# Kernel tuning notes

Hardware: AMD Instinct MI355X
Metric: run time of the kernel (lower is better)

Reference implementation:

```python
import jax, jax.numpy as jnp
import numpy as np

N_NODES = 50000
N_EDGES = 800000
IN_C, HID_C, LAT_C = 128, 64, 32
DEC_HID, REC_C = 64, 128


def _glorot(key, shape):
    fan_in, fan_out = shape
    lim = jnp.sqrt(6.0 / (fan_in + fan_out))
    return jax.random.uniform(key, shape, jnp.float32, -lim, lim)


def setup_inputs() -> dict:
    key = jax.random.key(0)
    ks = jax.random.split(key, 8)
    x = jax.random.normal(ks[0], (N_NODES, IN_C), jnp.float32)
    edge_index = jax.random.randint(ks[1], (2, N_EDGES), 0, N_NODES, jnp.int64 if jax.config.jax_enable_x64 else jnp.int32)
    return {
        "x": x,
        "edge_index": edge_index,
        "W_e1": _glorot(ks[2], (IN_C, HID_C)), "b_e1": jnp.zeros((HID_C,), jnp.float32),
        "W_e2": _glorot(ks[3], (HID_C, LAT_C)), "b_e2": jnp.zeros((LAT_C,), jnp.float32),
        "W_d1": _glorot(ks[4], (LAT_C, DEC_HID)), "b_d1": jnp.zeros((DEC_HID,), jnp.float32),
        "W_d2": _glorot(ks[5], (DEC_HID, REC_C)), "b_d2": jnp.zeros((REC_C,), jnp.float32),
    }


def _gcn_conv(x, src, dst, dinv, W, b, n_nodes):
    # GCNConv: h = D^{-1/2} (A + I) D^{-1/2} (x W) + b, expressed over the edge list
    h = x @ W                                   # [N, out]
    norm = dinv[src] * dinv[dst]                # [E+N] symmetric normalization
    msg = h[src] * norm[:, None]                # gather + per-edge scale (memory-bound)
    out = jax.ops.segment_sum(msg, dst, num_segments=n_nodes)  # scatter-add
    return out + b


def reference(x, edge_index, W_e1, b_e1, W_e2, b_e2, W_d1, b_d1, W_d2, b_d2):
    n = x.shape[0]
    loops = jnp.arange(n, dtype=edge_index.dtype)
    src = jnp.concatenate([edge_index[0], loops])
    dst = jnp.concatenate([edge_index[1], loops])
    # degree (with self-loops) computed once; deg >= 1 so rsqrt is safe
    deg = jax.ops.segment_sum(jnp.ones_like(src, dtype=x.dtype), dst, num_segments=n)
    dinv = jax.lax.rsqrt(deg)

    # encoder (dropout is eval-mode identity)
    h = jax.nn.relu(_gcn_conv(x, src, dst, dinv, W_e1, b_e1, n))
    z = _gcn_conv(h, src, dst, dinv, W_e2, b_e2, n)           # latent embeddings
    # decoder mirrors GCNConv layers
    d = jax.nn.relu(_gcn_conv(z, src, dst, dinv, W_d1, b_d1, n))
    x_rec = _gcn_conv(d, src, dst, dinv, W_d2, b_d2, n)       # [N, reconstructed_feature_dim]
    return x_rec
```

## Files before the change

### kernel.cpp

```cpp
#include <hip/hip_runtime.h>

typedef _Float16 half4 __attribute__((ext_vector_type(4)));
typedef _Float16 half8 __attribute__((ext_vector_type(8)));


static constexpr int NPB_SHIFT = 6;
static constexpr int NPB = 1 << NPB_SHIFT;
static constexpr int MAX_BKT = 1024;
static constexpr int PS_CHUNK = 4096;

__global__ __launch_bounds__(256) void hist_kernel(const int* __restrict__ dst, int E,
                                                   int nbkt, int* __restrict__ hist) {
    __shared__ int lc[MAX_BKT];
    int tid = threadIdx.x;
    int b = blockIdx.x;
    int e0 = b * PS_CHUNK;
    int e1 = e0 + PS_CHUNK; if (e1 > E) e1 = E;
    for (int i = tid; i < nbkt; i += 256) lc[i] = 0;
    __syncthreads();
    for (int i = e0 + tid; i < e1; i += 256)
        atomicAdd(&lc[dst[i] >> NPB_SHIFT], 1);
    __syncthreads();
    for (int i = tid; i < nbkt; i += 256) hist[(size_t)b * nbkt + i] = lc[i];
}

__global__ __launch_bounds__(256) void col_scan_kernel(int* __restrict__ hist, int nchunk,
                                                       int nbkt, int* __restrict__ bcnt) {
    int i = blockIdx.x * 4 + (threadIdx.x >> 6);
    if (i >= nbkt) return;
    int lane = threadIdx.x & 63;
    int run = 0;
    for (int c0 = 0; c0 < nchunk; c0 += 64) {
        int c = c0 + lane;
        int v = (c < nchunk) ? hist[(size_t)c * nbkt + i] : 0;
        int inc = v;
#pragma unroll
        for (int m = 1; m < 64; m <<= 1) {
            int u = __shfl_up(inc, m);
            if (lane >= m) inc += u;
        }
        if (c < nchunk) hist[(size_t)c * nbkt + i] = run + inc - v;
        run += __shfl(inc, 63);
    }
    if (lane == 0) bcnt[i] = run;
}

__global__ __launch_bounds__(256) void bucket_scan_kernel(const int* __restrict__ bcnt, int nbkt,
                                                          int* __restrict__ bbase,
                                                          int* __restrict__ rowp, int n) {
    __shared__ int wsum[4];
    int tid = threadIdx.x, lane = tid & 63, w = tid >> 6;
    int chunk = (nbkt + 255) / 256;
    int begin = tid * chunk;
    int end = begin + chunk; if (end > nbkt) end = nbkt;
    int s = 0;
    for (int i = begin; i < end; ++i) s += bcnt[i];
    int inc = s;
#pragma unroll
    for (int m = 1; m < 64; m <<= 1) {
        int u = __shfl_up(inc, m);
        if (lane >= m) inc += u;
    }
    if (lane == 63) wsum[w] = inc;
    __syncthreads();
    int off = 0;
    for (int i = 0; i < w; ++i) off += wsum[i];
    int run = off + inc - s;
    for (int i = begin; i < end; ++i) {
        bbase[i] = run;
        run += bcnt[i];
    }
    if (tid == 255) { bbase[nbkt] = run; rowp[n] = run; }
}

__global__ __launch_bounds__(256) void pair_blocksort_kernel(const int* __restrict__ src,
                                                             const int* __restrict__ dst,
                                                             int E, int nbkt,
                                                             const int* __restrict__ hist,
                                                             const int* __restrict__ bbase,
                                                             int* __restrict__ part) {
    __shared__ int2 pairs[PS_CHUNK];
    __shared__ int lbase[MAX_BKT];
    __shared__ int lcur[MAX_BKT];
    __shared__ int gpos[MAX_BKT];
    __shared__ int wsum[4];
    const int tid = threadIdx.x;
    const int b = blockIdx.x;
    const int e0 = b * PS_CHUNK;
    int e1 = e0 + PS_CHUNK; if (e1 > E) e1 = E;

    for (int i = tid; i < nbkt; i += 256) {
        lcur[i] = 0;
        gpos[i] = bbase[i] + hist[(size_t)b * nbkt + i];
    }
    __syncthreads();
    for (int i = e0 + tid; i < e1; i += 256)
        atomicAdd(&lcur[dst[i] >> NPB_SHIFT], 1);
    __syncthreads();
    {
        int b0 = tid * 4;
        int v[4]; int s = 0;
#pragma unroll
        for (int k = 0; k < 4; ++k) {
            int bb = b0 + k;
            v[k] = (bb < nbkt) ? lcur[bb] : 0;
            s += v[k];
        }
        int lane = tid & 63, w = tid >> 6;
        int inc = s;
#pragma unroll
        for (int m = 1; m < 64; m <<= 1) {
            int u = __shfl_up(inc, m);
            if (lane >= m) inc += u;
        }
        if (lane == 63) wsum[w] = inc;
        __syncthreads();
        int off = 0;
        for (int i = 0; i < w; ++i) off += wsum[i];
        int run = off + inc - s;
        __syncthreads();
#pragma unroll
        for (int k = 0; k < 4; ++k) {
            int bb = b0 + k;
            if (bb < nbkt) { lbase[bb] = run; lcur[bb] = run; }
            run += v[k];
        }
    }
    __syncthreads();
    for (int i = e0 + tid; i < e1; i += 256) {
        int s = src[i], d = dst[i];
        int p = atomicAdd(&lcur[d >> NPB_SHIFT], 1);
        pairs[p] = make_int2(s, d);
    }
    __syncthreads();
    const int cnt = e1 - e0;
    for (int i = tid; i < cnt; i += 256) {
        int2 pr = pairs[i];
        int bk = pr.y >> NPB_SHIFT;
        part[gpos[bk] + (i - lbase[bk])] = (pr.x << NPB_SHIFT) | (pr.y & (NPB - 1));
    }
}


template <bool HALF>
__device__ __forceinline__ float4 ldrow4(const void* H, size_t off) {
    if constexpr (HALF) {
        half4 h = *reinterpret_cast<const half4*>(reinterpret_cast<const _Float16*>(H) + off);
        return make_float4((float)h.x, (float)h.y, (float)h.z, (float)h.w);
    } else {
        return *reinterpret_cast<const float4*>(reinterpret_cast<const float*>(H) + off);
    }
}

template <bool HALF>
__device__ __forceinline__ void strow4(void* H, size_t off, float4 o) {
    if constexpr (HALF) {
        half4 hv;
        hv.x = (_Float16)o.x; hv.y = (_Float16)o.y;
        hv.z = (_Float16)o.z; hv.w = (_Float16)o.w;
        *reinterpret_cast<half4*>(reinterpret_cast<_Float16*>(H) + off) = hv;
    } else {
        *reinterpret_cast<float4*>(reinterpret_cast<float*>(H) + off) = o;
    }
}

__global__ __launch_bounds__(256) void csr_g1_kernel(
        const int* __restrict__ part, const int* __restrict__ bbase, int n,
        int* __restrict__ rowp, float* __restrict__ dinv, int* __restrict__ csr,
        const float* __restrict__ X, const float* __restrict__ We1,
        void* __restrict__ H1) {
    __shared__ int lcnt[NPB];
    __shared__ float sdinv[NPB];
    __shared__ __align__(16) char smem[50176];
    const int b = blockIdx.x, tid = threadIdx.x;
    const int node0 = b << NPB_SHIFT;
    int nloc = n - node0; if (nloc > NPB) nloc = NPB;
    const int p0 = bbase[b], p1 = bbase[b + 1];

    if (tid < NPB) lcnt[tid] = 0;
    __syncthreads();
    for (int i = p0 + tid; i < p1; i += 256)
        atomicAdd(&lcnt[part[i] & (NPB - 1)], 1);
    __syncthreads();
    if (tid < 64) {
        int c = lcnt[tid];
        int inc = c;
#pragma unroll
        for (int m = 1; m < 64; m <<= 1) {
            int u = __shfl_up(inc, m);
            if (tid >= m) inc += u;
        }
        int base = p0 + inc - c;
        float dv = rsqrtf((float)(c + 1));
        if (tid < nloc) {
            rowp[node0 + tid] = base;
            dinv[node0 + tid] = dv;
        }
        sdinv[tid] = dv;
        lcnt[tid] = base;
    }
    __syncthreads();
    for (int i = p0 + tid; i < p1; i += 256) {
        int w = part[i];
        int pos = atomicAdd(&lcnt[w & (NPB - 1)], 1);
        csr[pos] = w >> NPB_SHIFT;
    }
    __syncthreads();

    float (*At)[68] = reinterpret_cast<float (*)[68]>(smem);
    float (*Bl)[64] = reinterpret_cast<float (*)[64]>(smem + 17408);
    const int tx = tid % 16, ty = tid / 16;

    for (int i = tid; i < 128 * 16; i += 256) {
        int k = i / 16, c4 = (i % 16) * 4;
        *reinterpret_cast<float4*>(&Bl[k][c4]) =
            *reinterpret_cast<const float4*>(&We1[(size_t)k * 64 + c4]);
    }

    float acc[4][4] = {};
#pragma unroll
    for (int ch = 0; ch < 2; ++ch) {
        if (ch) __syncthreads();
        for (int i = tid; i < 64 * 16; i += 256) {
            int r = i / 16, k0 = (i % 16) * 4;
            int rg = node0 + r; if (rg > n - 1) rg = n - 1;
            float4 xv = *reinterpret_cast<const float4*>(&X[(size_t)rg * 128 + ch * 64 + k0]);
            At[k0 + 0][r] = xv.x;
            At[k0 + 1][r] = xv.y;
            At[k0 + 2][r] = xv.z;
            At[k0 + 3][r] = xv.w;
        }
        __syncthreads();
#pragma unroll 8
        for (int k = 0; k < 64; ++k) {
            float4 a = *reinterpret_cast<const float4*>(&At[k][ty * 4]);
            float4 bb = *reinterpret_cast<const float4*>(&Bl[ch * 64 + k][tx * 4]);
            acc[0][0] = fmaf(a.x, bb.x, acc[0][0]); acc[0][1] = fmaf(a.x, bb.y, acc[0][1]);
            acc[0][2] = fmaf(a.x, bb.z, acc[0][2]); acc[0][3] = fmaf(a.x, bb.w, acc[0][3]);
            acc[1][0] = fmaf(a.y, bb.x, acc[1][0]); acc[1][1] = fmaf(a.y, bb.y, acc[1][1]);
            acc[1][2] = fmaf(a.y, bb.z, acc[1][2]); acc[1][3] = fmaf(a.y, bb.w, acc[1][3]);
            acc[2][0] = fmaf(a.z, bb.x, acc[2][0]); acc[2][1] = fmaf(a.z, bb.y, acc[2][1]);
            acc[2][2] = fmaf(a.z, bb.z, acc[2][2]); acc[2][3] = fmaf(a.z, bb.w, acc[2][3]);
            acc[3][0] = fmaf(a.w, bb.x, acc[3][0]); acc[3][1] = fmaf(a.w, bb.y, acc[3][1]);
            acc[3][2] = fmaf(a.w, bb.z, acc[3][2]); acc[3][3] = fmaf(a.w, bb.w, acc[3][3]);
        }
    }
#pragma unroll
    for (int i = 0; i < 4; ++i) {
        int r = ty * 4 + i;
        int nd = node0 + r;
        if (nd < n) {
            float dv = sdinv[r];
            float4 o = make_float4(acc[i][0] * dv, acc[i][1] * dv,
                                   acc[i][2] * dv, acc[i][3] * dv);
            strow4<true>(H1, (size_t)nd * 64 + tx * 4, o);
        }
    }
}

template <int K, int OUT, int BN, bool BIAS, bool RELU, bool SCALE, bool HALF_IN, bool HALF_OUT>
__global__ __launch_bounds__(16 * (BN / 4)) void gemm_tile_kernel(
        const void* __restrict__ X, const float* __restrict__ W,
        const float* __restrict__ bias, const float* __restrict__ dinv,
        void* __restrict__ Hout, int n) {
    constexpr int BM = 64;
    constexpr int KB = (K > 64) ? 64 : K;
    constexpr int NTHR = 16 * (BN / 4);
    constexpr int KV = KB / 4;

    __shared__ float At[KB][BM + 4];
    __shared__ float Bl[K][BN];

    const int tid = threadIdx.x;
    const int tx = tid % (BN / 4);
    const int ty = tid / (BN / 4);
    const int rb = blockIdx.x * BM;
    const int co = blockIdx.y * BN;

    for (int i = tid; i < K * BN / 4; i += NTHR) {
        int k = i / (BN / 4);
        int c0 = (i % (BN / 4)) * 4;
        *reinterpret_cast<float4*>(&Bl[k][c0]) =
            *reinterpret_cast<const float4*>(&W[(size_t)k * OUT + co + c0]);
    }

    float acc[4][4] = {};

#pragma unroll
    for (int ch = 0; ch < K / KB; ++ch) {
        if (ch) __syncthreads();
        for (int i = tid; i < BM * KV; i += NTHR) {
            int r = i / KV;
            int k0 = (i % KV) * 4;
            int rg = rb + r; if (rg > n - 1) rg = n - 1;
            float4 xv = ldrow4<HALF_IN>(X, (size_t)rg * K + ch * KB + k0);
            At[k0 + 0][r] = xv.x;
            At[k0 + 1][r] = xv.y;
            At[k0 + 2][r] = xv.z;
            At[k0 + 3][r] = xv.w;
        }
        __syncthreads();

#pragma unroll 8
        for (int k = 0; k < KB; ++k) {
            float4 a = *reinterpret_cast<const float4*>(&At[k][ty * 4]);
            float4 b = *reinterpret_cast<const float4*>(&Bl[ch * KB + k][tx * 4]);
            acc[0][0] = fmaf(a.x, b.x, acc[0][0]); acc[0][1] = fmaf(a.x, b.y, acc[0][1]);
            acc[0][2] = fmaf(a.x, b.z, acc[0][2]); acc[0][3] = fmaf(a.x, b.w, acc[0][3]);
            acc[1][0] = fmaf(a.y, b.x, acc[1][0]); acc[1][1] = fmaf(a.y, b.y, acc[1][1]);
            acc[1][2] = fmaf(a.y, b.z, acc[1][2]); acc[1][3] = fmaf(a.y, b.w, acc[1][3]);
            acc[2][0] = fmaf(a.z, b.x, acc[2][0]); acc[2][1] = fmaf(a.z, b.y, acc[2][1]);
            acc[2][2] = fmaf(a.z, b.z, acc[2][2]); acc[2][3] = fmaf(a.z, b.w, acc[2][3]);
            acc[3][0] = fmaf(a.w, b.x, acc[3][0]); acc[3][1] = fmaf(a.w, b.y, acc[3][1]);
            acc[3][2] = fmaf(a.w, b.z, acc[3][2]); acc[3][3] = fmaf(a.w, b.w, acc[3][3]);
        }
    }

    float4 bv = make_float4(0.f, 0.f, 0.f, 0.f);
    if (BIAS) bv = *reinterpret_cast<const float4*>(&bias[co + tx * 4]);
    int r0 = rb + ty * 4;
#pragma unroll
    for (int i = 0; i < 4; ++i) {
        int r = r0 + i;
        if (r < n) {
            float4 o;
            o.x = acc[i][0]; o.y = acc[i][1]; o.z = acc[i][2]; o.w = acc[i][3];
            if (BIAS) { o.x += bv.x; o.y += bv.y; o.z += bv.z; o.w += bv.w; }
            if (RELU) {
                o.x = fmaxf(o.x, 0.f); o.y = fmaxf(o.y, 0.f);
                o.z = fmaxf(o.z, 0.f); o.w = fmaxf(o.w, 0.f);
            }
            if (SCALE) {
                float dv = dinv[r];
                o.x *= dv; o.y *= dv; o.z *= dv; o.w *= dv;
            }
            strow4<HALF_OUT>(Hout, (size_t)r * OUT + co + tx * 4, o);
        }
    }
}

template <int C, bool RELU, bool HAS_BIAS, bool POST_SCALE>
__global__ __launch_bounds__(256) void aggregate_kernel(const _Float16* __restrict__ H,
                                                        const int* __restrict__ row,
                                                        const int* __restrict__ csr_src,
                                                        const float* __restrict__ dinv,
                                                        const float* __restrict__ bias,
                                                        _Float16* __restrict__ Y, int n) {
    constexpr int LPN = C / 8;
    constexpr int EG = 64 / LPN;
    int wid = (blockIdx.x * blockDim.x + threadIdx.x) >> 6;
    if (wid >= n) return;
    int lane = threadIdx.x & 63;
    int g = lane / LPN;
    int c0 = (lane % LPN) * 8;
    const int node = wid;

    float accA[8] = {};
    float accB[8] = {};
    if (g == 0) {
        half8 h = *reinterpret_cast<const half8*>(H + (size_t)node * C + c0);
#pragma unroll
        for (int j = 0; j < 8; ++j) accA[j] = (float)h[j];
    }
    int e = row[node] + g;
    const int end = row[node + 1];
    for (; e + EG < end; e += 2 * EG) {
        int s0 = csr_src[e];
        int s1 = csr_src[e + EG];
        half8 h0 = *reinterpret_cast<const half8*>(H + (size_t)s0 * C + c0);
        half8 h1 = *reinterpret_cast<const half8*>(H + (size_t)s1 * C + c0);
#pragma unroll
        for (int j = 0; j < 8; ++j) { accA[j] += (float)h0[j]; accB[j] += (float)h1[j]; }
    }
    if (e < end) {
        int s = csr_src[e];
        half8 h = *reinterpret_cast<const half8*>(H + (size_t)s * C + c0);
#pragma unroll
        for (int j = 0; j < 8; ++j) accA[j] += (float)h[j];
    }
#pragma unroll
    for (int j = 0; j < 8; ++j) accA[j] += accB[j];
#pragma unroll
    for (int m = LPN; m < 64; m <<= 1) {
#pragma unroll
        for (int j = 0; j < 8; ++j) accA[j] += __shfl_xor(accA[j], m);
    }
    if (g == 0) {
        float dv = dinv[node];
        half8 o;
#pragma unroll
        for (int j = 0; j < 8; ++j) {
            float v = accA[j] * dv;
            if (HAS_BIAS) v += bias[c0 + j];
            if (RELU) v = fmaxf(v, 0.f);
            if (POST_SCALE) v *= dv;
            o[j] = (_Float16)v;
        }
        *reinterpret_cast<half8*>(Y + (size_t)node * C + c0) = o;
    }
}


static inline int cdiv(int a, int b) { return (a + b - 1) / b; }

extern "C" void kernel_launch(void* const* d_in, const int* in_sizes, int n_in,
                              void* d_out, int out_size, void* d_ws, size_t ws_size,
                              hipStream_t stream) {
    const float* x   = (const float*)d_in[0];
    const int*   ei  = (const int*)d_in[1];
    const float* We1 = (const float*)d_in[2];
    const float* be1 = (const float*)d_in[3];
    const float* We2 = (const float*)d_in[4];
    const float* be2 = (const float*)d_in[5];
    const float* Wd1 = (const float*)d_in[6];
    const float* bd1 = (const float*)d_in[7];
    const float* Wd2 = (const float*)d_in[8];
    const float* bd2 = (const float*)d_in[9];

    const int n = in_sizes[0] / 128;
    const int E = in_sizes[1] / 2;
    const int* src = ei;
    const int* dst = ei + E;
    const int nbkt = cdiv(n, NPB);
    const int nchunk = cdiv(E, PS_CHUNK);
    const int nrb = cdiv(n, 64);
    const int nwv = cdiv(n * 64, 256);

    char* ws = (char*)d_ws;
    auto carve = [&](size_t bytes) -> void* {
        void* p = (void*)ws;
        ws += (bytes + 255) & ~(size_t)255;
        return p;
    };
    int*   hist = (int*)carve((size_t)nchunk * nbkt * 4);
    int*   bcnt = (int*)carve((size_t)nbkt * 4);
    int*   bbase= (int*)carve((size_t)(nbkt + 1) * 4);
    int*   part = (int*)carve((size_t)E * 4);
    int*   rowp = (int*)carve((size_t)(n + 1) * 4);
    float* dinv = (float*)carve((size_t)n * 4);
    int*   csr  = (int*)carve((size_t)E * 4);
    _Float16* P1 = (_Float16*)carve((size_t)n * 64 * 2);
    _Float16* P2 = (_Float16*)carve((size_t)n * 64 * 2);
    _Float16* P3 = (_Float16*)carve((size_t)n * 32 * 2);
    _Float16* P4 = (_Float16*)carve((size_t)n * 32 * 2);

    hist_kernel<<<nchunk, 256, 0, stream>>>(dst, E, nbkt, hist);
    col_scan_kernel<<<cdiv(nbkt, 4), 256, 0, stream>>>(hist, nchunk, nbkt, bcnt);
    bucket_scan_kernel<<<1, 256, 0, stream>>>(bcnt, nbkt, bbase, rowp, n);
    pair_blocksort_kernel<<<nchunk, 256, 0, stream>>>(src, dst, E, nbkt, hist, bbase, part);

    csr_g1_kernel<<<nbkt, 256, 0, stream>>>(part, bbase, n, rowp, dinv, csr, x, We1, P1);

    aggregate_kernel<64, true, true, false>
        <<<nwv, 256, 0, stream>>>(P1, rowp, csr, dinv, be1, P2, n);

    gemm_tile_kernel<64, 32, 32, false, false, true, true, true>
        <<<dim3(nrb, 1), 128, 0, stream>>>(P2, We2, nullptr, dinv, P3, n);

    aggregate_kernel<32, false, true, true>
        <<<nwv, 256, 0, stream>>>(P3, rowp, csr, dinv, be2, P4, n);

    aggregate_kernel<32, false, false, false>
        <<<nwv, 256, 0, stream>>>(P4, rowp, csr, dinv, nullptr, P3, n);

    gemm_tile_kernel<32, 64, 64, true, true, true, true, true>
        <<<dim3(nrb, 1), 256, 0, stream>>>(P3, Wd1, bd1, dinv, P1, n);

    aggregate_kernel<64, false, false, false>
        <<<nwv, 256, 0, stream>>>(P1, rowp, csr, dinv, nullptr, P2, n);

    gemm_tile_kernel<64, 128, 64, true, false, false, true, false>
        <<<dim3(nrb, 2), 256, 0, stream>>>(P2, Wd2, bd2, dinv, d_out, n);
}
```

Baseline: 184.2 us.

## Fuse neighbor aggregation with following dense layer matmul per node

```diff
diff --git a/kernel.cpp b/kernel.cpp
--- a/kernel.cpp
+++ b/kernel.cpp
@@ -143,16 +143,6 @@
 
 
 template <bool HALF>
-__device__ __forceinline__ float4 ldrow4(const void* H, size_t off) {
-    if constexpr (HALF) {
-        half4 h = *reinterpret_cast<const half4*>(reinterpret_cast<const _Float16*>(H) + off);
-        return make_float4((float)h.x, (float)h.y, (float)h.z, (float)h.w);
-    } else {
-        return *reinterpret_cast<const float4*>(reinterpret_cast<const float*>(H) + off);
-    }
-}
-
-template <bool HALF>
 __device__ __forceinline__ void strow4(void* H, size_t off, float4 o) {
     if constexpr (HALF) {
         half4 hv;
@@ -254,87 +244,6 @@
             float4 o = make_float4(acc[i][0] * dv, acc[i][1] * dv,
                                    acc[i][2] * dv, acc[i][3] * dv);
             strow4<true>(H1, (size_t)nd * 64 + tx * 4, o);
-        }
-    }
-}
-
-template <int K, int OUT, int BN, bool BIAS, bool RELU, bool SCALE, bool HALF_IN, bool HALF_OUT>
-__global__ __launch_bounds__(16 * (BN / 4)) void gemm_tile_kernel(
-        const void* __restrict__ X, const float* __restrict__ W,
-        const float* __restrict__ bias, const float* __restrict__ dinv,
-        void* __restrict__ Hout, int n) {
-    constexpr int BM = 64;
-    constexpr int KB = (K > 64) ? 64 : K;
-    constexpr int NTHR = 16 * (BN / 4);
-    constexpr int KV = KB / 4;
-
-    __shared__ float At[KB][BM + 4];
-    __shared__ float Bl[K][BN];
-
-    const int tid = threadIdx.x;
-    const int tx = tid % (BN / 4);
-    const int ty = tid / (BN / 4);
-    const int rb = blockIdx.x * BM;
-    const int co = blockIdx.y * BN;
-
-    for (int i = tid; i < K * BN / 4; i += NTHR) {
-        int k = i / (BN / 4);
-        int c0 = (i % (BN / 4)) * 4;
-        *reinterpret_cast<float4*>(&Bl[k][c0]) =
-            *reinterpret_cast<const float4*>(&W[(size_t)k * OUT + co + c0]);
-    }
-
-    float acc[4][4] = {};
-
-#pragma unroll
-    for (int ch = 0; ch < K / KB; ++ch) {
-        if (ch) __syncthreads();
-        for (int i = tid; i < BM * KV; i += NTHR) {
-            int r = i / KV;
-            int k0 = (i % KV) * 4;
-            int rg = rb + r; if (rg > n - 1) rg = n - 1;
-            float4 xv = ldrow4<HALF_IN>(X, (size_t)rg * K + ch * KB + k0);
-            At[k0 + 0][r] = xv.x;
-            At[k0 + 1][r] = xv.y;
-            At[k0 + 2][r] = xv.z;
-            At[k0 + 3][r] = xv.w;
-        }
-        __syncthreads();
-
-#pragma unroll 8
-        for (int k = 0; k < KB; ++k) {
-            float4 a = *reinterpret_cast<const float4*>(&At[k][ty * 4]);
-            float4 b = *reinterpret_cast<const float4*>(&Bl[ch * KB + k][tx * 4]);
-            acc[0][0] = fmaf(a.x, b.x, acc[0][0]); acc[0][1] = fmaf(a.x, b.y, acc[0][1]);
-            acc[0][2] = fmaf(a.x, b.z, acc[0][2]); acc[0][3] = fmaf(a.x, b.w, acc[0][3]);
-            acc[1][0] = fmaf(a.y, b.x, acc[1][0]); acc[1][1] = fmaf(a.y, b.y, acc[1][1]);
-            acc[1][2] = fmaf(a.y, b.z, acc[1][2]); acc[1][3] = fmaf(a.y, b.w, acc[1][3]);
-            acc[2][0] = fmaf(a.z, b.x, acc[2][0]); acc[2][1] = fmaf(a.z, b.y, acc[2][1]);
-            acc[2][2] = fmaf(a.z, b.z, acc[2][2]); acc[2][3] = fmaf(a.z, b.w, acc[2][3]);
-            acc[3][0] = fmaf(a.w, b.x, acc[3][0]); acc[3][1] = fmaf(a.w, b.y, acc[3][1]);
-            acc[3][2] = fmaf(a.w, b.z, acc[3][2]); acc[3][3] = fmaf(a.w, b.w, acc[3][3]);
-        }
-    }
-
-    float4 bv = make_float4(0.f, 0.f, 0.f, 0.f);
-    if (BIAS) bv = *reinterpret_cast<const float4*>(&bias[co + tx * 4]);
-    int r0 = rb + ty * 4;
-#pragma unroll
-    for (int i = 0; i < 4; ++i) {
-        int r = r0 + i;
-        if (r < n) {
-            float4 o;
-            o.x = acc[i][0]; o.y = acc[i][1]; o.z = acc[i][2]; o.w = acc[i][3];
-            if (BIAS) { o.x += bv.x; o.y += bv.y; o.z += bv.z; o.w += bv.w; }
-            if (RELU) {
-                o.x = fmaxf(o.x, 0.f); o.y = fmaxf(o.y, 0.f);
-                o.z = fmaxf(o.z, 0.f); o.w = fmaxf(o.w, 0.f);
-            }
-            if (SCALE) {
-                float dv = dinv[r];
-                o.x *= dv; o.y *= dv; o.z *= dv; o.w *= dv;
-            }
-            strow4<HALF_OUT>(Hout, (size_t)r * OUT + co + tx * 4, o);
         }
     }
 }
@@ -400,6 +309,140 @@
     }
 }
 
+template <int CIN, int COUT, bool A_BIAS, bool A_RELU,
+          bool B_BIAS, bool B_RELU, bool B_SCALE, bool OUT_HALF>
+__global__ __launch_bounds__(256) void agg_mv_kernel(
+        const _Float16* __restrict__ H, const int* __restrict__ row,
+        const int* __restrict__ csr_src, const float* __restrict__ dinv,
+        const float* __restrict__ abias, const float* __restrict__ W,
+        const float* __restrict__ bbias, void* __restrict__ Out, int n) {
+    constexpr int LPN = CIN / 8;
+    constexpr int EG = 64 / LPN;
+    constexpr int WPAD = CIN + 8;
+    __shared__ __align__(16) _Float16 Wl[COUT][WPAD];
+    __shared__ __align__(16) _Float16 rowbuf[4][CIN];
+
+    const int tid = threadIdx.x;
+    for (int i = tid; i < CIN * COUT; i += 256) {
+        int k = i / COUT, c = i % COUT;
+        Wl[c][k] = (_Float16)W[(size_t)k * COUT + c];
+    }
+    __syncthreads();
+
+    const int wv = tid >> 6, lane = tid & 63;
+    const int node = blockIdx.x * 4 + wv;
+    if (node >= n) return;
+    const int g = lane / LPN;
+    const int c0 = (lane % LPN) * 8;
+
+    float accA[8] = {};
+    float accB[8] = {};
+    if (g == 0) {
+        half8 h = *reinterpret_cast<const half8*>(H + (size_t)node * CIN + c0);
+#pragma unroll
+        for (int j = 0; j < 8; ++j) accA[j] = (float)h[j];
+    }
+    int e = row[node] + g;
+    const int end = row[node + 1];
+    for (; e + EG < end; e += 2 * EG) {
+        int s0 = csr_src[e];
+        int s1 = csr_src[e + EG];
+        half8 h0 = *reinterpret_cast<const half8*>(H + (size_t)s0 * CIN + c0);
+        half8 h1 = *reinterpret_cast<const half8*>(H + (size_t)s1 * CIN + c0);
+#pragma unroll
+        for (int j = 0; j < 8; ++j) { accA[j] += (float)h0[j]; accB[j] += (float)h1[j]; }
+    }
+    if (e < end) {
+        int s = csr_src[e];
+        half8 h = *reinterpret_cast<const half8*>(H + (size_t)s * CIN + c0);
+#pragma unroll
+        for (int j = 0; j < 8; ++j) accA[j] += (float)h[j];
+    }
+#pragma unroll
+    for (int j = 0; j < 8; ++j) accA[j] += accB[j];
+#pragma unroll
+    for (int m = LPN; m < 64; m <<= 1) {
+#pragma unroll
+        for (int j = 0; j < 8; ++j) accA[j] += __shfl_xor(accA[j], m);
+    }
+
+    const float dv = dinv[node];
+    if (g == 0) {
+        half8 o;
+#pragma unroll
+        for (int j = 0; j < 8; ++j) {
+            float v = accA[j] * dv;
+            if (A_BIAS) v += abias[c0 + j];
+            if (A_RELU) v = fmaxf(v, 0.f);
+            o[j] = (_Float16)v;
+        }
+        *reinterpret_cast<half8*>(&rowbuf[wv][c0]) = o;
+    }
+    const _Float16* rb = rowbuf[wv];
+
+    if constexpr (COUT == 32) {
+        const int c = lane & 31, kh = lane >> 5;
+        float acc = 0.f;
+#pragma unroll
+        for (int kb = 0; kb < CIN / 16; ++kb) {
+            half8 r8 = *reinterpret_cast<const half8*>(rb + kh * (CIN / 2) + kb * 8);
+            half8 w8 = *reinterpret_cast<const half8*>(&Wl[c][kh * (CIN / 2) + kb * 8]);
+#pragma unroll
+            for (int j = 0; j < 8; ++j) acc = fmaf((float)r8[j], (float)w8[j], acc);
+        }
+        acc += __shfl_xor(acc, 32);
+        if (lane < 32) {
+            float v = acc;
+            if (B_BIAS) v += bbias[c];
+            if (B_RELU) v = fmaxf(v, 0.f);
+            if (B_SCALE) v *= dv;
+            if (OUT_HALF) ((_Float16*)Out)[(size_t)node * COUT + c] = (_Float16)v;
+            else          ((float*)Out)[(size_t)node * COUT + c] = v;
+        }
+    } else if constexpr (COUT == 64) {
+        const int c = lane;
+        float acc = 0.f;
+#pragma unroll
+        for (int kb = 0; kb < CIN / 8; ++kb) {
+            half8 r8 = *reinterpret_cast<const half8*>(rb + kb * 8);
+            half8 w8 = *reinterpret_cast<const half8*>(&Wl[c][kb * 8]);
+#pragma unroll
+            for (int j = 0; j < 8; ++j) acc = fmaf((float)r8[j], (float)w8[j], acc);
+        }
+        float v = acc;
+        if (B_BIAS) v += bbias[c];
+        if (B_RELU) v = fmaxf(v, 0.f);
+        if (B_SCALE) v *= dv;
+        if (OUT_HALF) ((_Float16*)Out)[(size_t)node * COUT + c] = (_Float16)v;
+        else          ((float*)Out)[(size_t)node * COUT + c] = v;
+    } else {
+        const int ca = lane, cb = lane + 64;
+        float a0 = 0.f, a1 = 0.f;
+#pragma unroll
+        for (int kb = 0; kb < CIN / 8; ++kb) {
+            half8 r8 = *reinterpret_cast<const half8*>(rb + kb * 8);
+            half8 w0 = *reinterpret_cast<const half8*>(&Wl[ca][kb * 8]);
+            half8 w1 = *reinterpret_cast<const half8*>(&Wl[cb][kb * 8]);
+#pragma unroll
+            for (int j = 0; j < 8; ++j) {
+                a0 = fmaf((float)r8[j], (float)w0[j], a0);
+                a1 = fmaf((float)r8[j], (float)w1[j], a1);
+            }
+        }
+        float v0 = a0, v1 = a1;
+        if (B_BIAS) { v0 += bbias[ca]; v1 += bbias[cb]; }
+        if (B_RELU) { v0 = fmaxf(v0, 0.f); v1 = fmaxf(v1, 0.f); }
+        if (B_SCALE) { v0 *= dv; v1 *= dv; }
+        if (OUT_HALF) {
+            ((_Float16*)Out)[(size_t)node * COUT + ca] = (_Float16)v0;
+            ((_Float16*)Out)[(size_t)node * COUT + cb] = (_Float16)v1;
+        } else {
+            ((float*)Out)[(size_t)node * COUT + ca] = v0;
+            ((float*)Out)[(size_t)node * COUT + cb] = v1;
+        }
+    }
+}
+
 
 static inline int cdiv(int a, int b) { return (a + b - 1) / b; }
 
@@ -423,8 +466,7 @@
     const int* dst = ei + E;
     const int nbkt = cdiv(n, NPB);
     const int nchunk = cdiv(E, PS_CHUNK);
-    const int nrb = cdiv(n, 64);
-    const int nwv = cdiv(n * 64, 256);
+    const int nwb = cdiv(n, 4);
 
     char* ws = (char*)d_ws;
     auto carve = [&](size_t bytes) -> void* {
@@ -440,7 +482,6 @@
     float* dinv = (float*)carve((size_t)n * 4);
     int*   csr  = (int*)carve((size_t)E * 4);
     _Float16* P1 = (_Float16*)carve((size_t)n * 64 * 2);
-    _Float16* P2 = (_Float16*)carve((size_t)n * 64 * 2);
     _Float16* P3 = (_Float16*)carve((size_t)n * 32 * 2);
     _Float16* P4 = (_Float16*)carve((size_t)n * 32 * 2);
 
@@ -451,24 +492,15 @@
 
     csr_g1_kernel<<<nbkt, 256, 0, stream>>>(part, bbase, n, rowp, dinv, csr, x, We1, P1);
 
-    aggregate_kernel<64, true, true, false>
-        <<<nwv, 256, 0, stream>>>(P1, rowp, csr, dinv, be1, P2, n);
-
-    gemm_tile_kernel<64, 32, 32, false, false, true, true, true>
-        <<<dim3(nrb, 1), 128, 0, stream>>>(P2, We2, nullptr, dinv, P3, n);
+    agg_mv_kernel<64, 32, true, true, false, false, true, true>
+        <<<nwb, 256, 0, stream>>>(P1, rowp, csr, dinv, be1, We2, nullptr, P3, n);
 
     aggregate_kernel<32, false, true, true>
-        <<<nwv, 256, 0, stream>>>(P3, rowp, csr, dinv, be2, P4, n);
-
-    aggregate_kernel<32, false, false, false>
-        <<<nwv, 256, 0, stream>>>(P4, rowp, csr, dinv, nullptr, P3, n);
-
-    gemm_tile_kernel<32, 64, 64, true, true, true, true, true>
-        <<<dim3(nrb, 1), 256, 0, stream>>>(P3, Wd1, bd1, dinv, P1, n);
-
-    aggregate_kernel<64, false, false, false>
-        <<<nwv, 256, 0, stream>>>(P1, rowp, csr, dinv, nullptr, P2, n);
-
-    gemm_tile_kernel<64, 128, 64, true, false, false, true, false>
-        <<<dim3(nrb, 2), 256, 0, stream>>>(P2, Wd2, bd2, dinv, d_out, n);
-}
+        <<<cdiv(n * 64, 256), 256, 0, stream>>>(P3, rowp, csr, dinv, be2, P4, n);
+
+    agg_mv_kernel<32, 64, false, false, true, true, true, true>
+        <<<nwb, 256, 0, stream>>>(P4, rowp, csr, dinv, nullptr, Wd1, bd1, P1, n);
+
+    agg_mv_kernel<64, 128, false, false, true, false, false, false>
+        <<<nwb, 256, 0, stream>>>(P1, rowp, csr, dinv, nullptr, Wd2, bd2, d_out, n);
+}
```

Result: slower. 201.2 us (+9.2%).

## Fuse neighbor aggregation with following small dense transform per node

Applied to the files above, without the earlier changes.

```diff
diff --git a/kernel.cpp b/kernel.cpp
--- a/kernel.cpp
+++ b/kernel.cpp
@@ -143,16 +143,6 @@
 
 
 template <bool HALF>
-__device__ __forceinline__ float4 ldrow4(const void* H, size_t off) {
-    if constexpr (HALF) {
-        half4 h = *reinterpret_cast<const half4*>(reinterpret_cast<const _Float16*>(H) + off);
-        return make_float4((float)h.x, (float)h.y, (float)h.z, (float)h.w);
-    } else {
-        return *reinterpret_cast<const float4*>(reinterpret_cast<const float*>(H) + off);
-    }
-}
-
-template <bool HALF>
 __device__ __forceinline__ void strow4(void* H, size_t off, float4 o) {
     if constexpr (HALF) {
         half4 hv;
@@ -254,87 +244,6 @@
             float4 o = make_float4(acc[i][0] * dv, acc[i][1] * dv,
                                    acc[i][2] * dv, acc[i][3] * dv);
             strow4<true>(H1, (size_t)nd * 64 + tx * 4, o);
-        }
-    }
-}
-
-template <int K, int OUT, int BN, bool BIAS, bool RELU, bool SCALE, bool HALF_IN, bool HALF_OUT>
-__global__ __launch_bounds__(16 * (BN / 4)) void gemm_tile_kernel(
-        const void* __restrict__ X, const float* __restrict__ W,
-        const float* __restrict__ bias, const float* __restrict__ dinv,
-        void* __restrict__ Hout, int n) {
-    constexpr int BM = 64;
-    constexpr int KB = (K > 64) ? 64 : K;
-    constexpr int NTHR = 16 * (BN / 4);
-    constexpr int KV = KB / 4;
-
-    __shared__ float At[KB][BM + 4];
-    __shared__ float Bl[K][BN];
-
-    const int tid = threadIdx.x;
-    const int tx = tid % (BN / 4);
-    const int ty = tid / (BN / 4);
-    const int rb = blockIdx.x * BM;
-    const int co = blockIdx.y * BN;
-
-    for (int i = tid; i < K * BN / 4; i += NTHR) {
-        int k = i / (BN / 4);
-        int c0 = (i % (BN / 4)) * 4;
-        *reinterpret_cast<float4*>(&Bl[k][c0]) =
-            *reinterpret_cast<const float4*>(&W[(size_t)k * OUT + co + c0]);
-    }
-
-    float acc[4][4] = {};
-
-#pragma unroll
-    for (int ch = 0; ch < K / KB; ++ch) {
-        if (ch) __syncthreads();
-        for (int i = tid; i < BM * KV; i += NTHR) {
-            int r = i / KV;
-            int k0 = (i % KV) * 4;
-            int rg = rb + r; if (rg > n - 1) rg = n - 1;
-            float4 xv = ldrow4<HALF_IN>(X, (size_t)rg * K + ch * KB + k0);
-            At[k0 + 0][r] = xv.x;
-            At[k0 + 1][r] = xv.y;
-            At[k0 + 2][r] = xv.z;
-            At[k0 + 3][r] = xv.w;
-        }
-        __syncthreads();
-
-#pragma unroll 8
-        for (int k = 0; k < KB; ++k) {
-            float4 a = *reinterpret_cast<const float4*>(&At[k][ty * 4]);
-            float4 b = *reinterpret_cast<const float4*>(&Bl[ch * KB + k][tx * 4]);
-            acc[0][0] = fmaf(a.x, b.x, acc[0][0]); acc[0][1] = fmaf(a.x, b.y, acc[0][1]);
-            acc[0][2] = fmaf(a.x, b.z, acc[0][2]); acc[0][3] = fmaf(a.x, b.w, acc[0][3]);
-            acc[1][0] = fmaf(a.y, b.x, acc[1][0]); acc[1][1] = fmaf(a.y, b.y, acc[1][1]);
-            acc[1][2] = fmaf(a.y, b.z, acc[1][2]); acc[1][3] = fmaf(a.y, b.w, acc[1][3]);
-            acc[2][0] = fmaf(a.z, b.x, acc[2][0]); acc[2][1] = fmaf(a.z, b.y, acc[2][1]);
-            acc[2][2] = fmaf(a.z, b.z, acc[2][2]); acc[2][3] = fmaf(a.z, b.w, acc[2][3]);
-            acc[3][0] = fmaf(a.w, b.x, acc[3][0]); acc[3][1] = fmaf(a.w, b.y, acc[3][1]);
-            acc[3][2] = fmaf(a.w, b.z, acc[3][2]); acc[3][3] = fmaf(a.w, b.w, acc[3][3]);
-        }
-    }
-
-    float4 bv = make_float4(0.f, 0.f, 0.f, 0.f);
-    if (BIAS) bv = *reinterpret_cast<const float4*>(&bias[co + tx * 4]);
-    int r0 = rb + ty * 4;
-#pragma unroll
-    for (int i = 0; i < 4; ++i) {
-        int r = r0 + i;
-        if (r < n) {
-            float4 o;
-            o.x = acc[i][0]; o.y = acc[i][1]; o.z = acc[i][2]; o.w = acc[i][3];
-            if (BIAS) { o.x += bv.x; o.y += bv.y; o.z += bv.z; o.w += bv.w; }
-            if (RELU) {
-                o.x = fmaxf(o.x, 0.f); o.y = fmaxf(o.y, 0.f);
-                o.z = fmaxf(o.z, 0.f); o.w = fmaxf(o.w, 0.f);
-            }
-            if (SCALE) {
-                float dv = dinv[r];
-                o.x *= dv; o.y *= dv; o.z *= dv; o.w *= dv;
-            }
-            strow4<HALF_OUT>(Hout, (size_t)r * OUT + co + tx * 4, o);
         }
     }
 }
@@ -400,6 +309,188 @@
     }
 }
 
+template <int CIN, int COUT, bool SPLITK, bool A_BIAS, bool A_RELU,
+          bool B_BIAS, bool B_RELU, bool B_SCALE>
+__global__ __launch_bounds__(256) void agg_mv_kernel(
+        const _Float16* __restrict__ H, const int* __restrict__ row,
+        const int* __restrict__ csr_src, const float* __restrict__ dinv,
+        const float* __restrict__ abias, const float* __restrict__ W,
+        const float* __restrict__ bbias, _Float16* __restrict__ Out, int n) {
+    constexpr int LPN = CIN / 8;
+    constexpr int EG = 64 / LPN;
+    __shared__ float Wf[CIN * COUT];
+    __shared__ float rowbuf[4][CIN];
+
+    const int tid = threadIdx.x;
+    for (int i = tid; i < CIN * COUT / 4; i += 256)
+        *reinterpret_cast<float4*>(&Wf[i * 4]) =
+            *reinterpret_cast<const float4*>(&W[i * 4]);
+    __syncthreads();
+
+    const int wv = tid >> 6, lane = tid & 63;
+    const int node = blockIdx.x * 4 + wv;
+    if (node >= n) return;
+    const int g = lane / LPN;
+    const int c0 = (lane % LPN) * 8;
+
+    float accA[8] = {};
+    float accB[8] = {};
+    if (g == 0) {
+        half8 h = *reinterpret_cast<const half8*>(H + (size_t)node * CIN + c0);
+#pragma unroll
+        for (int j = 0; j < 8; ++j) accA[j] = (float)h[j];
+    }
+    int e = row[node] + g;
+    const int end = row[node + 1];
+    for (; e + EG < end; e += 2 * EG) {
+        int s0 = csr_src[e];
+        int s1 = csr_src[e + EG];
+        half8 h0 = *reinterpret_cast<const half8*>(H + (size_t)s0 * CIN + c0);
+        half8 h1 = *reinterpret_cast<const half8*>(H + (size_t)s1 * CIN + c0);
+#pragma unroll
+        for (int j = 0; j < 8; ++j) { accA[j] += (float)h0[j]; accB[j] += (float)h1[j]; }
+    }
+    if (e < end) {
+        int s = csr_src[e];
+        half8 h = *reinterpret_cast<const half8*>(H + (size_t)s * CIN + c0);
+#pragma unroll
+        for (int j = 0; j < 8; ++j) accA[j] += (float)h[j];
+    }
+#pragma unroll
+    for (int j = 0; j < 8; ++j) accA[j] += accB[j];
+#pragma unroll
+    for (int m = LPN; m < 64; m <<= 1) {
+#pragma unroll
+        for (int j = 0; j < 8; ++j) accA[j] += __shfl_xor(accA[j], m);
+    }
+
+    const float dv = dinv[node];
+    if (g == 0) {
+        float4 lo, hi;
+        float v[8];
+#pragma unroll
+        for (int j = 0; j < 8; ++j) {
+            float t = accA[j] * dv;
+            if (A_BIAS) t += abias[c0 + j];
+            if (A_RELU) t = fmaxf(t, 0.f);
+            v[j] = t;
+        }
+        lo = make_float4(v[0], v[1], v[2], v[3]);
+        hi = make_float4(v[4], v[5], v[6], v[7]);
+        *reinterpret_cast<float4*>(&rowbuf[wv][c0]) = lo;
+        *reinterpret_cast<float4*>(&rowbuf[wv][c0 + 4]) = hi;
+    }
+    const float* rb = rowbuf[wv];
+
+    if constexpr (SPLITK) {
+        const int c = lane & 31, kh = lane >> 5;
+        float acc = 0.f;
+#pragma unroll
+        for (int k = 0; k < CIN / 2; ++k)
+            acc = fmaf(rb[kh * (CIN / 2) + k], Wf[(kh * (CIN / 2) + k) * COUT + c], acc);
+        acc += __shfl_xor(acc, 32);
+        if (lane < 32) {
+            float v = acc;
+            if (B_BIAS) v += bbias[c];
+            if (B_RELU) v = fmaxf(v, 0.f);
+            if (B_SCALE) v *= dv;
+            Out[(size_t)node * COUT + c] = (_Float16)v;
+        }
+    } else {
+        const int c = lane;
+        float acc = 0.f;
+#pragma unroll
+        for (int k = 0; k < CIN; ++k)
+            acc = fmaf(rb[k], Wf[k * COUT + c], acc);
+        float v = acc;
+        if (B_BIAS) v += bbias[c];
+        if (B_RELU) v = fmaxf(v, 0.f);
+        if (B_SCALE) v *= dv;
+        Out[(size_t)node * COUT + c] = (_Float16)v;
+    }
+}
+
+template <int K, int OUT, int BN, bool BIAS, bool RELU, bool SCALE>
+__global__ __launch_bounds__(16 * (BN / 4)) void gemm_tile_kernel(
+        const _Float16* __restrict__ X, const float* __restrict__ W,
+        const float* __restrict__ bias, const float* __restrict__ dinv,
+        float* __restrict__ Hout, int n) {
+    constexpr int BM = 64;
+    constexpr int KB = (K > 64) ? 64 : K;
+    constexpr int NTHR = 16 * (BN / 4);
+    constexpr int KV = KB / 4;
+
+    __shared__ float At[KB][BM + 4];
+    __shared__ float Bl[K][BN];
+
+    const int tid = threadIdx.x;
+    const int tx = tid % (BN / 4);
+    const int ty = tid / (BN / 4);
+    const int rb = blockIdx.x * BM;
+    const int co = blockIdx.y * BN;
+
+    for (int i = tid; i < K * BN / 4; i += NTHR) {
+        int k = i / (BN / 4);
+        int c0 = (i % (BN / 4)) * 4;
+        *reinterpret_cast<float4*>(&Bl[k][c0]) =
+            *reinterpret_cast<const float4*>(&W[(size_t)k * OUT + co + c0]);
+    }
+
+    float acc[4][4] = {};
+
+#pragma unroll
+    for (int ch = 0; ch < K / KB; ++ch) {
+        if (ch) __syncthreads();
+        for (int i = tid; i < BM * KV; i += NTHR) {
+            int r = i / KV;
+            int k0 = (i % KV) * 4;
+            int rg = rb + r; if (rg > n - 1) rg = n - 1;
+            half4 hv = *reinterpret_cast<const half4*>(&X[(size_t)rg * K + ch * KB + k0]);
+            At[k0 + 0][r] = (float)hv.x;
+            At[k0 + 1][r] = (float)hv.y;
+            At[k0 + 2][r] = (float)hv.z;
+            At[k0 + 3][r] = (float)hv.w;
+        }
+        __syncthreads();
+
+#pragma unroll 8
+        for (int k = 0; k < KB; ++k) {
+            float4 a = *reinterpret_cast<const float4*>(&At[k][ty * 4]);
+            float4 b = *reinterpret_cast<const float4*>(&Bl[ch * KB + k][tx * 4]);
+            acc[0][0] = fmaf(a.x, b.x, acc[0][0]); acc[0][1] = fmaf(a.x, b.y, acc[0][1]);
+            acc[0][2] = fmaf(a.x, b.z, acc[0][2]); acc[0][3] = fmaf(a.x, b.w, acc[0][3]);
+            acc[1][0] = fmaf(a.y, b.x, acc[1][0]); acc[1][1] = fmaf(a.y, b.y, acc[1][1]);
+            acc[1][2] = fmaf(a.y, b.z, acc[1][2]); acc[1][3] = fmaf(a.y, b.w, acc[1][3]);
+            acc[2][0] = fmaf(a.z, b.x, acc[2][0]); acc[2][1] = fmaf(a.z, b.y, acc[2][1]);
+            acc[2][2] = fmaf(a.z, b.z, acc[2][2]); acc[2][3] = fmaf(a.z, b.w, acc[2][3]);
+            acc[3][0] = fmaf(a.w, b.x, acc[3][0]); acc[3][1] = fmaf(a.w, b.y, acc[3][1]);
+            acc[3][2] = fmaf(a.w, b.z, acc[3][2]); acc[3][3] = fmaf(a.w, b.w, acc[3][3]);
+        }
+    }
+
+    float4 bv = make_float4(0.f, 0.f, 0.f, 0.f);
+    if (BIAS) bv = *reinterpret_cast<const float4*>(&bias[co + tx * 4]);
+    int r0 = rb + ty * 4;
+#pragma unroll
+    for (int i = 0; i < 4; ++i) {
+        int r = r0 + i;
+        if (r < n) {
+            float4 o;
+            o.x = acc[i][0]; o.y = acc[i][1]; o.z = acc[i][2]; o.w = acc[i][3];
+            if (BIAS) { o.x += bv.x; o.y += bv.y; o.z += bv.z; o.w += bv.w; }
+            if (RELU) {
+                o.x = fmaxf(o.x, 0.f); o.y = fmaxf(o.y, 0.f);
+                o.z = fmaxf(o.z, 0.f); o.w = fmaxf(o.w, 0.f);
+            }
+            if (SCALE) {
+                float dv = dinv[r];
+                o.x *= dv; o.y *= dv; o.z *= dv; o.w *= dv;
+            }
+            *reinterpret_cast<float4*>(&Hout[(size_t)r * OUT + co + tx * 4]) = o;
+        }
+    }
+}
+
 
 static inline int cdiv(int a, int b) { return (a + b - 1) / b; }
 
@@ -425,6 +516,7 @@
     const int nchunk = cdiv(E, PS_CHUNK);
     const int nrb = cdiv(n, 64);
     const int nwv = cdiv(n * 64, 256);
+    const int nwb = cdiv(n, 4);
 
     char* ws = (char*)d_ws;
     auto carve = [&](size_t bytes) -> void* {
@@ -451,24 +543,18 @@
 
     csr_g1_kernel<<<nbkt, 256, 0, stream>>>(part, bbase, n, rowp, dinv, csr, x, We1, P1);
 
-    aggregate_kernel<64, true, true, false>
-        <<<nwv, 256, 0, stream>>>(P1, rowp, csr, dinv, be1, P2, n);
-
-    gemm_tile_kernel<64, 32, 32, false, false, true, true, true>
-        <<<dim3(nrb, 1), 128, 0, stream>>>(P2, We2, nullptr, dinv, P3, n);
+    agg_mv_kernel<64, 32, true, true, true, false, false, true>
+        <<<nwb, 256, 0, stream>>>(P1, rowp, csr, dinv, be1, We2, nullptr, P3, n);
 
     aggregate_kernel<32, false, true, true>
         <<<nwv, 256, 0, stream>>>(P3, rowp, csr, dinv, be2, P4, n);
 
-    aggregate_kernel<32, false, false, false>
-        <<<nwv, 256, 0, stream>>>(P4, rowp, csr, dinv, nullptr, P3, n);
-
-    gemm_tile_kernel<32, 64, 64, true, true, true, true, true>
-        <<<dim3(nrb, 1), 256, 0, stream>>>(P3, Wd1, bd1, dinv, P1, n);
+    agg_mv_kernel<32, 64, false, false, false, true, true, true>
+        <<<nwb, 256, 0, stream>>>(P4, rowp, csr, dinv, nullptr, Wd1, bd1, P1, n);
 
     aggregate_kernel<64, false, false, false>
         <<<nwv, 256, 0, stream>>>(P1, rowp, csr, dinv, nullptr, P2, n);
 
-    gemm_tile_kernel<64, 128, 64, true, false, false, true, false>
-        <<<dim3(nrb, 2), 256, 0, stream>>>(P2, Wd2, bd2, dinv, d_out, n);
-}
+    gemm_tile_kernel<64, 128, 64, true, false, false>
+        <<<dim3(nrb, 2), 256, 0, stream>>>(P2, Wd2, bd2, dinv, (float*)d_out, n);
+}
```

New measurement: 193.8 us. 1.05x slower.
